# Kernel optimization log

Hardware: AMD Instinct MI355X
Metric: run time of the kernel (lower is better)

## Reference

```python
import jax, jax.numpy as jnp
import numpy as np

B, S, D, H = 4, 2048, 1024, 16
DH = D // H  # depth per head


def setup_inputs() -> dict:
    key = jax.random.key(0)
    ks = jax.random.split(key, 12)
    s = 1.0 / np.sqrt(D)
    return {
        "v": jax.random.normal(ks[0], (B, S, D), jnp.float32),
        "k": jax.random.normal(ks[1], (B, S, D), jnp.float32),
        "q": jax.random.normal(ks[2], (B, S, D), jnp.float32),
        "mask": jnp.ones((B, 1, S, S), jnp.float32),
        "wq_w": jax.random.normal(ks[3], (D, D), jnp.float32) * s,
        "wq_b": jnp.zeros((D,), jnp.float32),
        "wk_w": jax.random.normal(ks[4], (D, D), jnp.float32) * s,
        "wk_b": jnp.zeros((D,), jnp.float32),
        "wv_w": jax.random.normal(ks[5], (D, D), jnp.float32) * s,
        "wv_b": jnp.zeros((D,), jnp.float32),
        "wo_w": jax.random.normal(ks[6], (D, D), jnp.float32) * s,
        "wo_b": jnp.zeros((D,), jnp.float32),
    }


def _split_heads(x):
    # [B, S, D] -> [B, H, S, DH]
    b, s, _ = x.shape
    return x.reshape(b, s, H, DH).transpose(0, 2, 1, 3)


def reference(v, k, q, mask, wq_w, wq_b, wk_w, wk_b, wv_w, wv_b, wo_w, wo_b):
    qh = _split_heads(q @ wq_w + wq_b)
    kh = _split_heads(k @ wk_w + wk_b)
    vh = _split_heads(v @ wv_w + wv_b)
    # scaled dot-product attention with multiplicative custom mask
    logits = jnp.einsum("bhqd,bhkd->bhqk", qh, kh) / jnp.sqrt(jnp.float32(DH))
    logits = logits * mask - 1e6 * (1.0 - mask)
    attn_weights = jax.nn.softmax(logits, axis=-1)
    ctx = jnp.einsum("bhqk,bhkd->bhqd", attn_weights, vh)
    concat = ctx.transpose(0, 2, 1, 3).reshape(-1, q.shape[1], D)
    out = concat @ wo_w + wo_b
    return out, attn_weights
```

## Files before the change

kernel.cpp:

```cpp
#include <hip/hip_runtime.h>


typedef unsigned short u16;
typedef unsigned int   u32;
typedef u16   u16x4  __attribute__((ext_vector_type(4)));
typedef u16   u16x8  __attribute__((ext_vector_type(8)));
typedef int   i32x4  __attribute__((ext_vector_type(4)));
typedef float f32x4  __attribute__((ext_vector_type(4)));
typedef __bf16 bf16x8 __attribute__((ext_vector_type(8)));

#define GLDS16(gp, lp)                                                         \
  __builtin_amdgcn_global_load_lds(                                            \
      (const __attribute__((address_space(1))) void*)(gp),                     \
      (__attribute__((address_space(3))) void*)(lp), 16, 0, 0)

__device__ __forceinline__ u16 f2bf(float x) {
  __bf16 h = (__bf16)x;
  union { __bf16 h; u16 u; } c; c.h = h; return c.u;
}
__device__ __forceinline__ void nt_store4(float* p, f32x4 v) {
  __builtin_nontemporal_store(v, (f32x4*)p);
}

static const int Bn = 4, Sn = 2048, Dn = 1024, Hn = 16, DHn = 64;
#define MASK_NEG (-1442695.0f)

__global__ __launch_bounds__(256) void prep_k(
    const float* __restrict__ q, const float* __restrict__ k,
    const float* __restrict__ v, const float* __restrict__ mask,
    const float* __restrict__ w0, const float* __restrict__ w1,
    const float* __restrict__ w2, const float* __restrict__ w3,
    u16* __restrict__ qkv, u16* __restrict__ WTb, int* __restrict__ flags) {
  __shared__ __align__(16) u16 tile[64][72];
  __shared__ int ok_s;
  int bid = blockIdx.x, t = threadIdx.x;

  if (bid < 12288) {
    int which = bid >> 12;
    size_t li = (size_t)(bid & 4095) * 256 + t;
    const float* src = which == 0 ? q : which == 1 ? k : v;
    const f32x4* p = (const f32x4*)src + li * 2;
    f32x4 a = p[0], b = p[1];
    u16x8 r;
    r[0]=f2bf(a[0]); r[1]=f2bf(a[1]); r[2]=f2bf(a[2]); r[3]=f2bf(a[3]);
    r[4]=f2bf(b[0]); r[5]=f2bf(b[1]); r[6]=f2bf(b[2]); r[7]=f2bf(b[3]);
    *((u16x8*)(qkv + (size_t)which * 8388608) + li) = r;
  } else if (bid < 13312) {
    int i = bid - 12288;
    int z = i >> 8, rem = i & 255, bx = rem & 15, by = rem >> 4;
    const float* W = z == 0 ? w0 : z == 1 ? w1 : z == 2 ? w2 : w3;
    u16* WT = WTb + (size_t)z * 1048576;
    for (int rr = 0; rr < 4; rr++) {
      int r = rr * 16 + (t >> 4);
      int c = (t & 15) * 4;
      float4 vv = *(const float4*)(W + (size_t)(by * 64 + r) * 1024 + bx * 64 + c);
      tile[c + 0][r] = f2bf(vv.x); tile[c + 1][r] = f2bf(vv.y);
      tile[c + 2][r] = f2bf(vv.z); tile[c + 3][r] = f2bf(vv.w);
    }
    __syncthreads();
    for (int rr = 0; rr < 2; rr++) {
      int gid = rr * 256 + t;
      int r = gid >> 3, g = gid & 7;
      u16x8 vv = *(const u16x8*)&tile[r][g * 8];
      *(u16x8*)(WT + (size_t)(bx * 64 + r) * 1024 + by * 64 + g * 8) = vv;
    }
  } else {
    int i = bid - 13312;
    int qt = i & 15, kt = (i >> 4) & 31, b = i >> 9;
    if (t == 0) ok_s = 1;
    __syncthreads();
    const float* base = mask + ((size_t)b * Sn + qt * 128) * Sn + kt * 64;
    int r = t >> 1, c0 = (t & 1) * 32;
    const float* p = base + (size_t)r * Sn + c0;
    bool ok = true;
    for (int j = 0; j < 8; j++) {
      float4 vv = *(const float4*)(p + j * 4);
      ok = ok && (vv.x == 1.0f) && (vv.y == 1.0f) && (vv.z == 1.0f) && (vv.w == 1.0f);
    }
    if (!ok) atomicAnd(&ok_s, 0);
    __syncthreads();
    if (t == 0) flags[(b * 32 + kt) * 16 + qt] = ok_s;
  }
}

__device__ __forceinline__ void gemm_body(const u16* __restrict__ A,
                                          const u16* __restrict__ BT,
                                          const float* __restrict__ bias,
                                          void* __restrict__ outp, int mode,
                                          int nt, int mt, char* sm) {
  const int K = 1024;
  int m0 = mt * 128, n0 = nt * 128;
  int tid = threadIdx.x, w = tid >> 6, l = tid & 63, l15 = l & 15, l4 = l >> 4;
  int wm = w >> 1, wn = w & 1;

  size_t goff_a[4], goff_b[4];
  int lbase[4];
  for (int i = 0; i < 4; i++) {
    int gi = (w * 4 + i) * 64 + l;
    int row = gi >> 3, g = gi & 7;
    int gx = g ^ (row & 7);
    goff_a[i] = (size_t)(m0 + row) * K + gx * 8;
    goff_b[i] = (size_t)(n0 + row) * K + gx * 8;
    lbase[i] = (w * 4 + i) * 1024;
  }

  f32x4 acc[4][4] = {};
  for (int t = 0; t < 16; t++) {
    int k0 = t * 64;
    for (int i = 0; i < 4; i++) {
      GLDS16(A + goff_a[i] + k0, sm + lbase[i]);
      GLDS16(BT + goff_b[i] + k0, sm + 16384 + lbase[i]);
    }
    __syncthreads();
#pragma unroll
    for (int kk = 0; kk < 2; kk++) {
      int kb = kk * 64 + l4 * 16;
      bf16x8 af[4], bf[4];
#pragma unroll
      for (int mi = 0; mi < 4; mi++) {
        int row = wm * 64 + mi * 16 + l15;
        af[mi] = *(const bf16x8*)(sm + row * 128 + (kb ^ ((row & 7) << 4)));
      }
#pragma unroll
      for (int nj = 0; nj < 4; nj++) {
        int row = wn * 64 + nj * 16 + l15;
        bf[nj] = *(const bf16x8*)(sm + 16384 + row * 128 + (kb ^ ((row & 7) << 4)));
      }
#pragma unroll
      for (int mi = 0; mi < 4; mi++)
#pragma unroll
        for (int nj = 0; nj < 4; nj++)
          acc[mi][nj] = __builtin_amdgcn_mfma_f32_16x16x32_bf16(af[mi], bf[nj], acc[mi][nj], 0, 0, 0);
    }
    __syncthreads();
  }

  if (mode == 3) {
    float* out = (float*)outp;
#pragma unroll
    for (int mi = 0; mi < 4; mi++)
#pragma unroll
      for (int nj = 0; nj < 4; nj++)
#pragma unroll
        for (int r = 0; r < 4; r++) {
          int mg = m0 + wm * 64 + mi * 16 + l4 * 4 + r;
          int ng = n0 + wn * 64 + nj * 16 + l15;
          __builtin_nontemporal_store(acc[mi][nj][r] + bias[ng],
                                      out + (size_t)mg * 1024 + ng);
        }
  } else if (mode == 2) {
    u16* vt = (u16*)outp;
#pragma unroll
    for (int mi = 0; mi < 4; mi++)
#pragma unroll
      for (int nj = 0; nj < 4; nj++) {
        int col = wn * 64 + nj * 16 + l15;
        int rowb = wm * 64 + mi * 16 + l4 * 4;
        float bs = bias[n0 + col];
        u16x4 pk;
#pragma unroll
        for (int r = 0; r < 4; r++) pk[r] = f2bf(acc[mi][nj][r] + bs);
        *(u16x4*)(sm + col * 256 + (((rowb >> 3) * 16) ^ ((col & 7) << 4)) + (rowb & 7) * 2) = pk;
      }
    __syncthreads();
#pragma unroll
    for (int pass = 0; pass < 8; pass++) {
      int idx = pass * 256 + tid;
      int g = idx & 15, col = idx >> 4;
      i32x4 v = *(const i32x4*)(sm + col * 256 + ((g * 16) ^ ((col & 7) << 4)));
      int ng = n0 + col, h = ng >> 6, d = ng & 63;
      int mgb = m0 + g * 8, b = mgb >> 11, s = mgb & 2047;
      *(i32x4*)(vt + ((size_t)(b * Hn + h) * DHn + d) * Sn + s) = v;
    }
  } else {
    u16* oh = (u16*)outp;
    float sc = (mode == 0) ? 0.18033688f : 1.0f;
#pragma unroll
    for (int mi = 0; mi < 4; mi++)
#pragma unroll
      for (int nj = 0; nj < 4; nj++) {
        int col = wn * 64 + nj * 16 + l15;
        float bs = bias[n0 + col];
#pragma unroll
        for (int r = 0; r < 4; r++) {
          int row = wm * 64 + mi * 16 + l4 * 4 + r;
          *(u16*)(sm + row * 256 + (((col >> 3) * 16) ^ ((row & 7) << 4)) + (col & 7) * 2) =
              f2bf((acc[mi][nj][r] + bs) * sc);
        }
      }
    __syncthreads();
#pragma unroll
    for (int pass = 0; pass < 8; pass++) {
      int idx = pass * 256 + tid;
      int g = idx & 7, half = (idx >> 3) & 1, row = idx >> 4;
      i32x4 v = *(const i32x4*)(sm + row * 256 + (((half * 8 + g) * 16) ^ ((row & 7) << 4)));
      int hg = (n0 >> 6) + half;
      int mg = m0 + row, b = mg >> 11, s = mg & 2047;
      *(i32x4*)(oh + ((size_t)(b * Hn + hg) * Sn + s) * DHn + g * 8) = v;
    }
  }
}

__global__ __launch_bounds__(256) void gemmO_k(const u16* __restrict__ A,
                                               const u16* __restrict__ BT,
                                               const float* __restrict__ bias,
                                               float* __restrict__ outp) {
  __shared__ __align__(16) char sm[32768];
  int hw = blockIdx.x;
  int lg = (hw & 7) * 64 + (hw >> 3);
  int nt = lg & 7, mt = lg >> 3;
  gemm_body(A, BT, bias, (void*)outp, 3, nt, mt, sm);
}

__global__ __launch_bounds__(256) void gemm3_k(const u16* __restrict__ Ab,
                                               const u16* __restrict__ BTb,
                                               const float* __restrict__ b0,
                                               const float* __restrict__ b1,
                                               const float* __restrict__ b2,
                                               u16* __restrict__ outb) {
  __shared__ __align__(16) char sm[32768];
  int hw = blockIdx.x;
  int lg = (hw & 7) * 192 + (hw >> 3);
  int z = lg >> 9, r = lg & 511;
  int nt = r & 7, mt = r >> 3;
  const u16* A = Ab + (size_t)z * 8388608;
  const u16* BT = BTb + (size_t)z * 1048576;
  const float* bias = z == 0 ? b0 : z == 1 ? b1 : b2;
  u16* out = outb + (size_t)z * 8388608;
  gemm_body(A, BT, bias, (void*)out, z, nt, mt, sm);
}

#define K0_OFF 0
#define K1_OFF 8192
#define V0_OFF 16384
#define V1_OFF 24576
#define P_OFF  32768

__global__ __launch_bounds__(256) void attn_k(
    const u16* __restrict__ qh, const u16* __restrict__ kh,
    const u16* __restrict__ vt, const float* __restrict__ mask,
    const int* __restrict__ flags, float* __restrict__ attn,
    u16* __restrict__ ctxc) {
  __shared__ __align__(16) char sm[49152];
  int hw = blockIdx.x;
  int lg = (hw & 7) * 128 + (hw >> 3);
  int qt = lg & 15, h = (lg >> 4) & 15, b = lg >> 8;
  int bh = b * Hn + h;
  int tid = threadIdx.x, w = tid >> 6, l = tid & 63, l15 = l & 15, l4 = l >> 4;

  const u16* Qg = qh + ((size_t)bh * Sn + qt * 128) * DHn;
  const u16* Kg = kh + (size_t)bh * Sn * DHn;
  const u16* Vg = vt + (size_t)bh * DHn * Sn;
  const float* Mg = mask + (size_t)b * Sn * Sn + (size_t)(qt * 128) * Sn;

  u32 fl = (u32)__ballot(l < 32 && flags[(b * 32 + l) * 16 + qt] != 0);

  int srowA[4], sgxA[4], sdstA[4];
  for (int i = 0; i < 4; i++) {
    int gid = i * 256 + tid, row = gid >> 3, g = gid & 7;
    srowA[i] = row; sgxA[i] = (g ^ (row & 7)) * 8; sdstA[i] = gid * 16;
  }
#define STAGE_KA(t, buf)                                                       \
  for (int i = 0; i < 4; i++)                                                  \
    GLDS16(Kg + (size_t)((t) * 128 + srowA[i]) * DHn + sgxA[i], sm + (buf) + sdstA[i]);
#define STAGE_K(t, buf)                                                        \
  for (int i = 0; i < 2; i++)                                                  \
    GLDS16(Kg + (size_t)((t) * 64 + srowA[i]) * DHn + sgxA[i], sm + (buf) + sdstA[i]);
#define STAGE_V(t, buf)                                                        \
  for (int i = 0; i < 2; i++)                                                  \
    GLDS16(Vg + (size_t)srowA[i] * Sn + (t) * 64 + sgxA[i], sm + (buf) + sdstA[i]);

  bf16x8 qf[2][2];
#pragma unroll
  for (int ni = 0; ni < 2; ni++)
#pragma unroll
    for (int kk = 0; kk < 2; kk++)
      qf[ni][kk] = *(const bf16x8*)(Qg + (size_t)(w * 32 + ni * 16 + l15) * DHn + kk * 32 + l4 * 8);

  float lsum[2] = {0.f, 0.f};
  STAGE_KA(0, 0);
  for (int t = 0; t < 16; t++) {
    int kcur = (t & 1) ? 16384 : 0;
    __syncthreads();
    if (t < 15) { int knxt = (t & 1) ? 0 : 16384; STAGE_KA(t + 1, knxt); }
#pragma unroll
    for (int h2 = 0; h2 < 2; h2++) {
      int kt = t * 2 + h2;
      f32x4 s[4][2] = {};
#pragma unroll
      for (int kk = 0; kk < 2; kk++) {
        int kb = kk * 64 + l4 * 16;
        bf16x8 a[4];
#pragma unroll
        for (int mi = 0; mi < 4; mi++) {
          int row = h2 * 64 + mi * 16 + l15;
          a[mi] = *(const bf16x8*)(sm + kcur + row * 128 + (kb ^ ((row & 7) << 4)));
        }
#pragma unroll
        for (int mi = 0; mi < 4; mi++)
#pragma unroll
          for (int ni = 0; ni < 2; ni++)
            s[mi][ni] = __builtin_amdgcn_mfma_f32_16x16x32_bf16(a[mi], qf[ni][kk], s[mi][ni], 0, 0, 0);
      }
      if (!((fl >> kt) & 1)) {
#pragma unroll
        for (int ni = 0; ni < 2; ni++) {
          const float* mrow = Mg + (size_t)(w * 32 + ni * 16 + l15) * Sn + kt * 64;
#pragma unroll
          for (int mi = 0; mi < 4; mi++) {
            f32x4 mv = *(const f32x4*)(mrow + mi * 16 + l4 * 4);
#pragma unroll
            for (int r = 0; r < 4; r++)
              s[mi][ni][r] = s[mi][ni][r] * mv[r] + MASK_NEG * (1.f - mv[r]);
          }
        }
      }
#pragma unroll
      for (int ni = 0; ni < 2; ni++)
#pragma unroll
        for (int mi = 0; mi < 4; mi++)
#pragma unroll
          for (int r = 0; r < 4; r++) lsum[ni] += __builtin_exp2f(s[mi][ni][r]);
    }
  }
  float cv[2];
#pragma unroll
  for (int ni = 0; ni < 2; ni++) {
    lsum[ni] += __shfl_xor(lsum[ni], 16);
    lsum[ni] += __shfl_xor(lsum[ni], 32);
    cv[ni] = __builtin_log2f(lsum[ni]);
  }

  __syncthreads();
  f32x4 ctx[4][2] = {};
  STAGE_K(0, K0_OFF);
  STAGE_V(0, V0_OFF);
  for (int t = 0; t < 32; t++) {
    int kcur = (t & 1) ? K1_OFF : K0_OFF;
    int vcur = (t & 1) ? V1_OFF : V0_OFF;
    __syncthreads();
    if (t < 31) {
      int knxt = (t & 1) ? K0_OFF : K1_OFF;
      int vnxt = (t & 1) ? V0_OFF : V1_OFF;
      STAGE_K(t + 1, knxt);
      STAGE_V(t + 1, vnxt);
    }
    f32x4 s[4][2] = {};
#pragma unroll
    for (int kk = 0; kk < 2; kk++) {
      int kb = kk * 64 + l4 * 16;
      bf16x8 a[4];
#pragma unroll
      for (int mi = 0; mi < 4; mi++) {
        int row = mi * 16 + l15;
        a[mi] = *(const bf16x8*)(sm + kcur + row * 128 + (kb ^ ((row & 7) << 4)));
      }
#pragma unroll
      for (int mi = 0; mi < 4; mi++)
#pragma unroll
        for (int ni = 0; ni < 2; ni++)
          s[mi][ni] = __builtin_amdgcn_mfma_f32_16x16x32_bf16(a[mi], qf[ni][kk], s[mi][ni], 0, 0, 0);
    }
    if (!((fl >> t) & 1)) {
#pragma unroll
      for (int ni = 0; ni < 2; ni++) {
        const float* mrow = Mg + (size_t)(w * 32 + ni * 16 + l15) * Sn + t * 64;
#pragma unroll
        for (int mi = 0; mi < 4; mi++) {
          f32x4 mv = *(const f32x4*)(mrow + mi * 16 + l4 * 4);
#pragma unroll
          for (int r = 0; r < 4; r++)
            s[mi][ni][r] = s[mi][ni][r] * mv[r] + MASK_NEG * (1.f - mv[r]);
        }
      }
    }
#pragma unroll
    for (int ni = 0; ni < 2; ni++)
#pragma unroll
      for (int mi = 0; mi < 4; mi++)
#pragma unroll
        for (int r = 0; r < 4; r++) s[mi][ni][r] = __builtin_exp2f(s[mi][ni][r] - cv[ni]);
#pragma unroll
    for (int ni = 0; ni < 2; ni++) {
      float* arow = attn + ((size_t)bh * Sn + qt * 128 + w * 32 + ni * 16 + l15) * Sn + t * 64;
#pragma unroll
      for (int mi = 0; mi < 4; mi++)
        nt_store4(arow + mi * 16 + l4 * 4, s[mi][ni]);
    }
#pragma unroll
    for (int ni = 0; ni < 2; ni++) {
      int q = w * 32 + ni * 16 + l15;
#pragma unroll
      for (int mi = 0; mi < 4; mi++) {
        u16x4 pk;
#pragma unroll
        for (int r = 0; r < 4; r++) pk[r] = f2bf(s[mi][ni][r]);
        int kb = mi * 32 + l4 * 8;
        *(u16x4*)(sm + P_OFF + q * 128 + (kb ^ ((q & 7) << 4))) = pk;
      }
    }
#pragma unroll
    for (int kk = 0; kk < 2; kk++) {
      int kb = kk * 64 + l4 * 16;
      bf16x8 av[4], bp[2];
#pragma unroll
      for (int mi = 0; mi < 4; mi++) {
        int row = mi * 16 + l15;
        av[mi] = *(const bf16x8*)(sm + vcur + row * 128 + (kb ^ ((row & 7) << 4)));
      }
#pragma unroll
      for (int ni = 0; ni < 2; ni++) {
        int q = w * 32 + ni * 16 + l15;
        bp[ni] = *(const bf16x8*)(sm + P_OFF + q * 128 + (kb ^ ((q & 7) << 4)));
      }
#pragma unroll
      for (int mi = 0; mi < 4; mi++)
#pragma unroll
        for (int ni = 0; ni < 2; ni++)
          ctx[mi][ni] = __builtin_amdgcn_mfma_f32_16x16x32_bf16(av[mi], bp[ni], ctx[mi][ni], 0, 0, 0);
    }
  }

#pragma unroll
  for (int ni = 0; ni < 2; ni++) {
    int q = w * 32 + ni * 16 + l15;
#pragma unroll
    for (int mi = 0; mi < 4; mi++) {
      u16x4 ck;
#pragma unroll
      for (int r = 0; r < 4; r++) ck[r] = f2bf(ctx[mi][ni][r]);
      int db = mi * 32 + l4 * 8;
      *(u16x4*)(sm + P_OFF + q * 128 + (db ^ ((q & 7) << 4))) = ck;
    }
  }
  __syncthreads();
  {
    int q = tid >> 1, hf = tid & 1;
    u16* dst = ctxc + ((size_t)b * Sn + qt * 128 + q) * Dn + h * DHn + hf * 32;
#pragma unroll
    for (int c4 = 0; c4 < 4; c4++) {
      int db = hf * 64 + c4 * 16;
      i32x4 v = *(const i32x4*)(sm + P_OFF + q * 128 + (db ^ ((q & 7) << 4)));
      *(i32x4*)(dst + c4 * 8) = v;
    }
  }
}

extern "C" void kernel_launch(void* const* d_in, const int* in_sizes, int n_in,
                              void* d_out, int out_size, void* d_ws, size_t ws_size,
                              hipStream_t stream) {
  const float* v_f  = (const float*)d_in[0];
  const float* k_f  = (const float*)d_in[1];
  const float* q_f  = (const float*)d_in[2];
  const float* mask = (const float*)d_in[3];
  const float* wq_w = (const float*)d_in[4];
  const float* wq_b = (const float*)d_in[5];
  const float* wk_w = (const float*)d_in[6];
  const float* wk_b = (const float*)d_in[7];
  const float* wv_w = (const float*)d_in[8];
  const float* wv_b = (const float*)d_in[9];
  const float* wo_w = (const float*)d_in[10];
  const float* wo_b = (const float*)d_in[11];

  char* ws = (char*)d_ws;
  u16*   qbf  = (u16*)(ws + 0);
  u16*   wT   = (u16*)(ws + 50331648);
  u16*   woT  = (u16*)(ws + 56623104);
  u16*   qhp  = (u16*)(ws + 58720256);
  u16*   khp  = (u16*)(ws + 75497472);
  u16*   vtp  = (u16*)(ws + 92274688);
  u16*   ctxc = (u16*)(ws + 109051904);
  int*   flg  = (int*)(ws + 125829120);

  float* out  = (float*)d_out;
  float* attn = out + (size_t)Bn * Sn * Dn;

  prep_k<<<15360, 256, 0, stream>>>(q_f, k_f, v_f, mask,
                                    wq_w, wk_w, wv_w, wo_w, qbf, wT, flg);
  gemm3_k<<<1536, 256, 0, stream>>>(qbf, wT, wq_b, wk_b, wv_b, qhp);
  attn_k<<<1024, 256, 0, stream>>>(qhp, khp, vtp, mask, flg, attn, ctxc);
  gemmO_k<<<512, 256, 0, stream>>>(ctxc, woT, wo_b, out);
}
```

Before: 558.5 us.

## Halve attention query tile to 64 rows, doubling grid and cutting registers

Each attention block now handles 64 query rows instead of 128, with one 16-row query fragment per wave instead of two. The grid doubles to 2048 blocks and shared memory drops to 40 KB. The aim is lower register and LDS pressure for higher occupancy and better load balance across CUs. The cost is that each K/V tile loaded into LDS is reused by half as many queries, which doubles K/V traffic and halves MFMA work per LDS read.

```diff
diff --git a/kernel.cpp b/kernel.cpp
--- a/kernel.cpp
+++ b/kernel.cpp
@@ -241,19 +241,20 @@
     const u16* __restrict__ vt, const float* __restrict__ mask,
     const int* __restrict__ flags, float* __restrict__ attn,
     u16* __restrict__ ctxc) {
-  __shared__ __align__(16) char sm[49152];
+  __shared__ __align__(16) char sm[40960];
   int hw = blockIdx.x;
-  int lg = (hw & 7) * 128 + (hw >> 3);
-  int qt = lg & 15, h = (lg >> 4) & 15, b = lg >> 8;
+  int lg = (hw & 7) * 256 + (hw >> 3);
+  int qt = lg & 31, h = (lg >> 5) & 15, b = lg >> 9;
   int bh = b * Hn + h;
   int tid = threadIdx.x, w = tid >> 6, l = tid & 63, l15 = l & 15, l4 = l >> 4;
-
-  const u16* Qg = qh + ((size_t)bh * Sn + qt * 128) * DHn;
+  int qrow = w * 16 + l15;
+
+  const u16* Qg = qh + ((size_t)bh * Sn + qt * 64) * DHn;
   const u16* Kg = kh + (size_t)bh * Sn * DHn;
   const u16* Vg = vt + (size_t)bh * DHn * Sn;
-  const float* Mg = mask + (size_t)b * Sn * Sn + (size_t)(qt * 128) * Sn;
-
-  u32 fl = (u32)__ballot(l < 32 && flags[(b * 32 + l) * 16 + qt] != 0);
+  const float* Mg = mask + (size_t)b * Sn * Sn + (size_t)(qt * 64) * Sn;
+
+  u32 fl = (u32)__ballot(l < 32 && flags[(b * 32 + l) * 16 + (qt >> 1)] != 0);
 
   int srowA[4], sgxA[4], sdstA[4];
   for (int i = 0; i < 4; i++) {
@@ -270,14 +271,12 @@
   for (int i = 0; i < 2; i++)                                                  \
     GLDS16(Vg + (size_t)srowA[i] * Sn + (t) * 64 + sgxA[i], sm + (buf) + sdstA[i]);
 
-  bf16x8 qf[2][2];
-#pragma unroll
-  for (int ni = 0; ni < 2; ni++)
-#pragma unroll
-    for (int kk = 0; kk < 2; kk++)
-      qf[ni][kk] = *(const bf16x8*)(Qg + (size_t)(w * 32 + ni * 16 + l15) * DHn + kk * 32 + l4 * 8);
-
-  float lsum[2] = {0.f, 0.f};
+  bf16x8 qf[2];
+#pragma unroll
+  for (int kk = 0; kk < 2; kk++)
+    qf[kk] = *(const bf16x8*)(Qg + (size_t)qrow * DHn + kk * 32 + l4 * 8);
+
+  float lsum = 0.f;
   STAGE_KA(0, 0);
   for (int t = 0; t < 16; t++) {
     int kcur = (t & 1) ? 16384 : 0;
@@ -286,7 +285,7 @@
 #pragma unroll
     for (int h2 = 0; h2 < 2; h2++) {
       int kt = t * 2 + h2;
-      f32x4 s[4][2] = {};
+      f32x4 s[4] = {};
 #pragma unroll
       for (int kk = 0; kk < 2; kk++) {
         int kb = kk * 64 + l4 * 16;
@@ -298,41 +297,30 @@
         }
 #pragma unroll
         for (int mi = 0; mi < 4; mi++)
-#pragma unroll
-          for (int ni = 0; ni < 2; ni++)
-            s[mi][ni] = __builtin_amdgcn_mfma_f32_16x16x32_bf16(a[mi], qf[ni][kk], s[mi][ni], 0, 0, 0);
+          s[mi] = __builtin_amdgcn_mfma_f32_16x16x32_bf16(a[mi], qf[kk], s[mi], 0, 0, 0);
       }
       if (!((fl >> kt) & 1)) {
-#pragma unroll
-        for (int ni = 0; ni < 2; ni++) {
-          const float* mrow = Mg + (size_t)(w * 32 + ni * 16 + l15) * Sn + kt * 64;
-#pragma unroll
-          for (int mi = 0; mi < 4; mi++) {
-            f32x4 mv = *(const f32x4*)(mrow + mi * 16 + l4 * 4);
-#pragma unroll
-            for (int r = 0; r < 4; r++)
-              s[mi][ni][r] = s[mi][ni][r] * mv[r] + MASK_NEG * (1.f - mv[r]);
-          }
+        const float* mrow = Mg + (size_t)qrow * Sn + kt * 64;
+#pragma unroll
+        for (int mi = 0; mi < 4; mi++) {
+          f32x4 mv = *(const f32x4*)(mrow + mi * 16 + l4 * 4);
+#pragma unroll
+          for (int r = 0; r < 4; r++)
+            s[mi][r] = s[mi][r] * mv[r] + MASK_NEG * (1.f - mv[r]);
         }
       }
 #pragma unroll
-      for (int ni = 0; ni < 2; ni++)
-#pragma unroll
-        for (int mi = 0; mi < 4; mi++)
-#pragma unroll
-          for (int r = 0; r < 4; r++) lsum[ni] += __builtin_exp2f(s[mi][ni][r]);
-    }
-  }
-  float cv[2];
-#pragma unroll
-  for (int ni = 0; ni < 2; ni++) {
-    lsum[ni] += __shfl_xor(lsum[ni], 16);
-    lsum[ni] += __shfl_xor(lsum[ni], 32);
-    cv[ni] = __builtin_log2f(lsum[ni]);
-  }
+      for (int mi = 0; mi < 4; mi++)
+#pragma unroll
+        for (int r = 0; r < 4; r++) lsum += __builtin_exp2f(s[mi][r]);
+    }
+  }
+  lsum += __shfl_xor(lsum, 16);
+  lsum += __shfl_xor(lsum, 32);
+  float cv = __builtin_log2f(lsum);
 
   __syncthreads();
-  f32x4 ctx[4][2] = {};
+  f32x4 ctx[4] = {};
   STAGE_K(0, K0_OFF);
   STAGE_V(0, V0_OFF);
   for (int t = 0; t < 32; t++) {
@@ -345,7 +333,7 @@
       STAGE_K(t + 1, knxt);
       STAGE_V(t + 1, vnxt);
     }
-    f32x4 s[4][2] = {};
+    f32x4 s[4] = {};
 #pragma unroll
     for (int kk = 0; kk < 2; kk++) {
       int kb = kk * 64 + l4 * 16;
@@ -357,92 +345,68 @@
       }
 #pragma unroll
       for (int mi = 0; mi < 4; mi++)
-#pragma unroll
-        for (int ni = 0; ni < 2; ni++)
-          s[mi][ni] = __builtin_amdgcn_mfma_f32_16x16x32_bf16(a[mi], qf[ni][kk], s[mi][ni], 0, 0, 0);
+        s[mi] = __builtin_amdgcn_mfma_f32_16x16x32_bf16(a[mi], qf[kk], s[mi], 0, 0, 0);
     }
     if (!((fl >> t) & 1)) {
-#pragma unroll
-      for (int ni = 0; ni < 2; ni++) {
-        const float* mrow = Mg + (size_t)(w * 32 + ni * 16 + l15) * Sn + t * 64;
-#pragma unroll
-        for (int mi = 0; mi < 4; mi++) {
-          f32x4 mv = *(const f32x4*)(mrow + mi * 16 + l4 * 4);
-#pragma unroll
-          for (int r = 0; r < 4; r++)
-            s[mi][ni][r] = s[mi][ni][r] * mv[r] + MASK_NEG * (1.f - mv[r]);
-        }
-      }
-    }
-#pragma unroll
-    for (int ni = 0; ni < 2; ni++)
+      const float* mrow = Mg + (size_t)qrow * Sn + t * 64;
+#pragma unroll
+      for (int mi = 0; mi < 4; mi++) {
+        f32x4 mv = *(const f32x4*)(mrow + mi * 16 + l4 * 4);
+#pragma unroll
+        for (int r = 0; r < 4; r++)
+          s[mi][r] = s[mi][r] * mv[r] + MASK_NEG * (1.f - mv[r]);
+      }
+    }
+#pragma unroll
+    for (int mi = 0; mi < 4; mi++)
+#pragma unroll
+      for (int r = 0; r < 4; r++) s[mi][r] = __builtin_exp2f(s[mi][r] - cv);
+    {
+      float* arow = attn + ((size_t)bh * Sn + qt * 64 + qrow) * Sn + t * 64;
 #pragma unroll
       for (int mi = 0; mi < 4; mi++)
-#pragma unroll
-        for (int r = 0; r < 4; r++) s[mi][ni][r] = __builtin_exp2f(s[mi][ni][r] - cv[ni]);
-#pragma unroll
-    for (int ni = 0; ni < 2; ni++) {
-      float* arow = attn + ((size_t)bh * Sn + qt * 128 + w * 32 + ni * 16 + l15) * Sn + t * 64;
-#pragma unroll
-      for (int mi = 0; mi < 4; mi++)
-        nt_store4(arow + mi * 16 + l4 * 4, s[mi][ni]);
-    }
-#pragma unroll
-    for (int ni = 0; ni < 2; ni++) {
-      int q = w * 32 + ni * 16 + l15;
-#pragma unroll
-      for (int mi = 0; mi < 4; mi++) {
-        u16x4 pk;
-#pragma unroll
-        for (int r = 0; r < 4; r++) pk[r] = f2bf(s[mi][ni][r]);
-        int kb = mi * 32 + l4 * 8;
-        *(u16x4*)(sm + P_OFF + q * 128 + (kb ^ ((q & 7) << 4))) = pk;
-      }
+        nt_store4(arow + mi * 16 + l4 * 4, s[mi]);
+    }
+#pragma unroll
+    for (int mi = 0; mi < 4; mi++) {
+      u16x4 pk;
+#pragma unroll
+      for (int r = 0; r < 4; r++) pk[r] = f2bf(s[mi][r]);
+      int kb = mi * 32 + l4 * 8;
+      *(u16x4*)(sm + P_OFF + qrow * 128 + (kb ^ ((qrow & 7) << 4))) = pk;
     }
 #pragma unroll
     for (int kk = 0; kk < 2; kk++) {
       int kb = kk * 64 + l4 * 16;
-      bf16x8 av[4], bp[2];
+      bf16x8 av[4];
 #pragma unroll
       for (int mi = 0; mi < 4; mi++) {
         int row = mi * 16 + l15;
         av[mi] = *(const bf16x8*)(sm + vcur + row * 128 + (kb ^ ((row & 7) << 4)));
       }
-#pragma unroll
-      for (int ni = 0; ni < 2; ni++) {
-        int q = w * 32 + ni * 16 + l15;
-        bp[ni] = *(const bf16x8*)(sm + P_OFF + q * 128 + (kb ^ ((q & 7) << 4)));
-      }
+      bf16x8 bp = *(const bf16x8*)(sm + P_OFF + qrow * 128 + (kb ^ ((qrow & 7) << 4)));
 #pragma unroll
       for (int mi = 0; mi < 4; mi++)
-#pragma unroll
-        for (int ni = 0; ni < 2; ni++)
-          ctx[mi][ni] = __builtin_amdgcn_mfma_f32_16x16x32_bf16(av[mi], bp[ni], ctx[mi][ni], 0, 0, 0);
-    }
-  }
-
-#pragma unroll
-  for (int ni = 0; ni < 2; ni++) {
-    int q = w * 32 + ni * 16 + l15;
-#pragma unroll
-    for (int mi = 0; mi < 4; mi++) {
-      u16x4 ck;
-#pragma unroll
-      for (int r = 0; r < 4; r++) ck[r] = f2bf(ctx[mi][ni][r]);
-      int db = mi * 32 + l4 * 8;
-      *(u16x4*)(sm + P_OFF + q * 128 + (db ^ ((q & 7) << 4))) = ck;
-    }
+        ctx[mi] = __builtin_amdgcn_mfma_f32_16x16x32_bf16(av[mi], bp, ctx[mi], 0, 0, 0);
+    }
+  }
+
+#pragma unroll
+  for (int mi = 0; mi < 4; mi++) {
+    u16x4 ck;
+#pragma unroll
+    for (int r = 0; r < 4; r++) ck[r] = f2bf(ctx[mi][r]);
+    int db = mi * 32 + l4 * 8;
+    *(u16x4*)(sm + P_OFF + qrow * 128 + (db ^ ((qrow & 7) << 4))) = ck;
   }
   __syncthreads();
-  {
-    int q = tid >> 1, hf = tid & 1;
-    u16* dst = ctxc + ((size_t)b * Sn + qt * 128 + q) * Dn + h * DHn + hf * 32;
-#pragma unroll
-    for (int c4 = 0; c4 < 4; c4++) {
-      int db = hf * 64 + c4 * 16;
-      i32x4 v = *(const i32x4*)(sm + P_OFF + q * 128 + (db ^ ((q & 7) << 4)));
-      *(i32x4*)(dst + c4 * 8) = v;
-    }
+#pragma unroll
+  for (int pass = 0; pass < 2; pass++) {
+    int idx = pass * 256 + tid;
+    int g = idx & 7, q = idx >> 3;
+    i32x4 v = *(const i32x4*)(sm + P_OFF + q * 128 + ((g * 16) ^ ((q & 7) << 4)));
+    u16* dst = ctxc + ((size_t)b * Sn + qt * 64 + q) * Dn + h * DHn + g * 8;
+    *(i32x4*)dst = v;
   }
 }
 
@@ -478,6 +442,6 @@
   prep_k<<<15360, 256, 0, stream>>>(q_f, k_f, v_f, mask,
                                     wq_w, wk_w, wv_w, wo_w, qbf, wT, flg);
   gemm3_k<<<1536, 256, 0, stream>>>(qbf, wT, wq_b, wk_b, wv_b, qhp);
-  attn_k<<<1024, 256, 0, stream>>>(qhp, khp, vtp, mask, flg, attn, ctxc);
+  attn_k<<<2048, 256, 0, stream>>>(qhp, khp, vtp, mask, flg, attn, ctxc);
   gemmO_k<<<512, 256, 0, stream>>>(ctxc, woT, wo_b, out);
 }
```

Measured after the change: 558.4 us. About the same (-0.0%).
